# Kernel tuning notes

Measured on AMD Instinct MI355X. Metric: run time of the kernel, lower is better.

The kernel has to match this reference:

```python
import jax, jax.numpy as jnp
import numpy as np
from jax import lax

B, W, S, D, H, BH, C = 32, 128, 192, 768, 10, 30, 50
NEG = -1e30  # stand-in for -inf to keep grads NaN-free


def _lstm_dir(x, Wih, Whh, bih, bhh, reverse):
    # x: [B, T, D] -> [B, T, H]; torch gate order i, f, g, o
    xg = jnp.einsum('btd,gd->btg', x, Wih) + bih  # [B, T, 4H]
    if reverse:
        xg = xg[:, ::-1]

    def step(carry, g_t):
        h, c = carry
        g = g_t + h @ Whh.T + bhh
        i, f, gg, o = jnp.split(g, 4, axis=-1)
        c = jax.nn.sigmoid(f) * c + jax.nn.sigmoid(i) * jnp.tanh(gg)
        h = jax.nn.sigmoid(o) * jnp.tanh(c)
        return (h, c), h

    init = (jnp.zeros((x.shape[0], H), x.dtype), jnp.zeros((x.shape[0], H), x.dtype))
    _, hs = lax.scan(step, init, xg.transpose(1, 0, 2))
    hs = hs.transpose(1, 0, 2)
    if reverse:
        hs = hs[:, ::-1]
    return hs


def _biaffine(x, W1, b1, W2, b2, U, bias):
    # DeepBiaffineScorer: MLP+ReLU on each side, bilinear with bias-augmented inputs
    h1 = jax.nn.relu(x @ W1 + b1)
    h2 = jax.nn.relu(x @ W2 + b2)
    ones = jnp.ones(h1.shape[:-1] + (1,), h1.dtype)
    h1a = jnp.concatenate([h1, ones], -1)  # [B, W, BH+1]
    h2a = jnp.concatenate([h2, ones], -1)
    return jnp.einsum('bih,ohg,bjg->bijo', h1a, U, h2a) + bias  # [B, W, W, O]


def _ce_sum(logits, targets, ignore):
    # cross-entropy, reduction='sum', with ignore_index; classes on last axis
    logp = jax.nn.log_softmax(logits, -1)
    valid = targets != ignore
    t = jnp.where(valid, targets, 0)
    picked = jnp.take_along_axis(logp, t[..., None], -1).squeeze(-1)
    return -jnp.sum(jnp.where(valid, picked, 0.0))


def _forward(hiddens, bert2toks, heads, dep_rels, masks,
             Wih_f, Whh_f, bih_f, bhh_f, Wih_b, Whh_b, bih_b, bhh_b,
             un_W1, un_b1, un_W2, un_b2, un_U, un_bias,
             dr_W1, dr_b1, dr_W2, dr_b2, dr_U, dr_bias):
    # mean of the 3 selected BERT layers, then ragged subtoken -> word mean pooling
    means = jnp.mean(hiddens, axis=0)  # [B, S+1, D]
    sub = means[:, 1:]                 # skip [CLS]: [B, S, D]
    seg_sum = jax.vmap(lambda x, s: jax.ops.segment_sum(x, s, num_segments=W))(sub, bert2toks)
    cnt = jax.vmap(lambda s: jax.ops.segment_sum(jnp.ones((S,), sub.dtype), s, num_segments=W))(bert2toks)
    bert_out = seg_sum / jnp.maximum(cnt, 1.0)[..., None]  # [B, W, D]

    # BiLSTM (sent_lens are all full length W, so packing is the identity)
    fwd = _lstm_dir(bert_out, Wih_f, Whh_f, bih_f, bhh_f, False)
    bwd = _lstm_dir(bert_out, Wih_b, Whh_b, bih_b, bhh_b, True)
    unpacked = jnp.concatenate([fwd, bwd], -1)  # [B, W, 2H]

    unlabeled = _biaffine(unpacked, un_W1, un_b1, un_W2, un_b2, un_U, un_bias)[..., 0]  # [B, W, W]
    deprel = _biaffine(unpacked, dr_W1, dr_b1, dr_W2, dr_b2, dr_U, dr_bias)             # [B, W, W, C]

    eye = jnp.eye(W, dtype=bool)
    unlabeled = jnp.where(eye[None], NEG, unlabeled)

    # gather gold-head deprel scores: [B, W, C]
    head_scores = jnp.take_along_axis(deprel, heads[:, :, None, None], axis=2).squeeze(2)
    heads_ = jnp.where(masks, -1, heads)

    deprel_loss = _ce_sum(head_scores, dep_rels, 0)
    depind_loss = _ce_sum(unlabeled[:, 1:], heads_[:, 1:], -1)
    return deprel_loss + depind_loss


def setup_inputs() -> dict:
    key = jax.random.key(0)
    ks = jax.random.split(key, 26)
    hiddens = jax.random.normal(ks[0], (3, B, S + 1, D), jnp.float32)
    # non-decreasing subtoken->word map covering all W words
    bert2toks = jnp.broadcast_to((jnp.arange(S) * W) // S, (B, S)).astype(jnp.int32)
    heads = jax.random.randint(ks[1], (B, W), 0, W)
    heads = jnp.where(heads == jnp.arange(W)[None, :], 0, heads)  # no self-head (diag is -inf)
    dep_rels = jax.random.randint(ks[2], (B, W), 0, C)
    masks = jnp.zeros((B, W), bool)
    sent_lens = jnp.full((B,), W, jnp.int32)
    s = 0.1
    p = lambda k, shape: jax.random.normal(k, shape, jnp.float32) * s
    return dict(
        hiddens=hiddens, bert2toks=bert2toks, heads=heads, dep_rels=dep_rels,
        masks=masks, sent_lens=sent_lens,
        Wih_f=p(ks[3], (4 * H, D)), Whh_f=p(ks[4], (4 * H, H)), bih_f=p(ks[5], (4 * H,)), bhh_f=p(ks[6], (4 * H,)),
        Wih_b=p(ks[7], (4 * H, D)), Whh_b=p(ks[8], (4 * H, H)), bih_b=p(ks[9], (4 * H,)), bhh_b=p(ks[10], (4 * H,)),
        un_W1=p(ks[11], (2 * H, BH)), un_b1=p(ks[12], (BH,)), un_W2=p(ks[13], (2 * H, BH)), un_b2=p(ks[14], (BH,)),
        un_U=p(ks[15], (1, BH + 1, BH + 1)), un_bias=p(ks[16], (1,)),
        dr_W1=p(ks[17], (2 * H, BH)), dr_b1=p(ks[18], (BH,)), dr_W2=p(ks[19], (2 * H, BH)), dr_b2=p(ks[20], (BH,)),
        dr_U=p(ks[21], (C, BH + 1, BH + 1)), dr_bias=p(ks[22], (C,)),
    )


def reference(hiddens, bert2toks, heads, dep_rels, masks, sent_lens,
              Wih_f, Whh_f, bih_f, bhh_f, Wih_b, Whh_b, bih_b, bhh_b,
              un_W1, un_b1, un_W2, un_b2, un_U, un_bias,
              dr_W1, dr_b1, dr_W2, dr_b2, dr_U, dr_bias):
    # sent_lens unused: all sentences are full length, so pack/unpack is identity
    return _forward(hiddens, bert2toks, heads, dep_rels, masks,
                    Wih_f, Whh_f, bih_f, bhh_f, Wih_b, Whh_b, bih_b, bhh_b,
                    un_W1, un_b1, un_W2, un_b2, un_U, un_bias,
                    dr_W1, dr_b1, dr_W2, dr_b2, dr_U, dr_bias)
```

## Files before the change

kernel.cpp:

```cpp
#include <hip/hip_runtime.h>

#define Bn 32
#define Wn 128
#define Sn 192
#define Dn 768
#define Hn 10
#define BHn 30
#define Cn 50
#define CAP 8
#define NEGV -1e30f

__device__ __forceinline__ float fsig(float x) {
    return __builtin_amdgcn_rcpf(1.0f + __expf(-x));
}
__device__ __forceinline__ float ftanh(float x) {
    return 1.0f - 2.0f * __builtin_amdgcn_rcpf(1.0f + __expf(2.0f * x));
}
__device__ __forceinline__ float lane_bcast(float v, int srclane) {
    union { float f; int i; } u, w;
    u.f = v;
    w.i = __builtin_amdgcn_readlane(u.i, srclane);
    return w.f;
}
template <int Q>
__device__ __forceinline__ float quad_bcast(float v) {
    union { float f; int i; } u, w;
    u.f = v;
    w.i = __builtin_amdgcn_mov_dpp(u.i, (Q << 6) | (Q << 4) | (Q << 2) | Q, 0xf, 0xf, true);
    return w.f;
}

__global__ void k_zero(int* cnt, float* out) {
    int i = blockIdx.x * blockDim.x + threadIdx.x;
    if (i < Bn * Wn) cnt[i] = 0;
    if (i == 0) out[0] = 0.f;
}

__global__ void k_lists(const int* __restrict__ b2t, int* cnt, int* lists) {
    int idx = blockIdx.x * blockDim.x + threadIdx.x;
    if (idx >= Bn * Sn) return;
    int b = idx / Sn;
    int w = b2t[idx];
    if (w < 0 || w >= Wn) return;
    int s = idx % Sn;
    int pos = atomicAdd(&cnt[b * Wn + w], 1);
    if (pos < CAP) lists[(b * Wn + w) * CAP + pos] = s;
}

#define XSTR 100
#define WSTR 52
__global__ __launch_bounds__(256) void k_tokproj(const float* __restrict__ hid,
                                                 const float* __restrict__ Wf,
                                                 const float* __restrict__ Wb,
                                                 float* __restrict__ tokg4) {
    __shared__ float xl[64 * XSTR];
    __shared__ float wl[80 * WSTR];
    int tb = blockIdx.x >> 3;
    int kq = blockIdx.x & 7;
    int b = tb / 3;
    int s0 = (tb % 3) * 64;
    int k0 = kq * 96;
    int tid = threadIdx.x;

    for (int idx = tid; idx < 64 * 24; idx += 256) {
        int r = idx / 24, k4 = idx % 24;
        size_t rowbase = ((size_t)b * (Sn + 1) + (s0 + r + 1)) * Dn + k0 + 4 * k4;
        float4 v0 = *(const float4*)(hid + rowbase);
        float4 v1 = *(const float4*)(hid + (size_t)Bn * (Sn + 1) * Dn + rowbase);
        float4 v2 = *(const float4*)(hid + (size_t)2 * Bn * (Sn + 1) * Dn + rowbase);
        float4 v;
        v.x = v0.x + v1.x + v2.x; v.y = v0.y + v1.y + v2.y;
        v.z = v0.z + v1.z + v2.z; v.w = v0.w + v1.w + v2.w;
        *(float4*)(xl + r * XSTR + 4 * k4) = v;
    }

    int tg = tid >> 4;
    int rg = tid & 15;
    float acc[4][5];
#pragma unroll
    for (int tt = 0; tt < 4; ++tt)
#pragma unroll
        for (int rr = 0; rr < 5; ++rr) acc[tt][rr] = 0.f;

    for (int c = 0; c < 2; ++c) {
        __syncthreads();
        for (int idx = tid; idx < 80 * 12; idx += 256) {
            int co = idx / 12, k4c = idx % 12;
            int dir = co / 40, off = co % 40;
            int j = off >> 2, g = off & 3;
            const float* src = (dir ? Wb : Wf) + (g * 10 + j) * Dn + k0 + c * 48 + 4 * k4c;
            *(float4*)(wl + co * WSTR + 4 * k4c) = *(const float4*)src;
        }
        __syncthreads();
#pragma unroll 2
        for (int k4c = 0; k4c < 12; ++k4c) {
            float4 xv[4], wv[5];
#pragma unroll
            for (int tt = 0; tt < 4; ++tt)
                xv[tt] = *(const float4*)(xl + (tg * 4 + tt) * XSTR + c * 48 + 4 * k4c);
#pragma unroll
            for (int rr = 0; rr < 5; ++rr)
                wv[rr] = *(const float4*)(wl + (rg * 5 + rr) * WSTR + 4 * k4c);
#pragma unroll
            for (int tt = 0; tt < 4; ++tt)
#pragma unroll
                for (int rr = 0; rr < 5; ++rr) {
                    acc[tt][rr] += xv[tt].x * wv[rr].x + xv[tt].y * wv[rr].y
                                 + xv[tt].z * wv[rr].z + xv[tt].w * wv[rr].w;
                }
        }
    }
    size_t nbase = (size_t)kq * (Bn * Sn) + (size_t)b * Sn + s0;
#pragma unroll
    for (int tt = 0; tt < 4; ++tt) {
        size_t ob = (nbase + tg * 4 + tt) * 80 + rg * 5;
#pragma unroll
        for (int rr = 0; rr < 5; ++rr) tokg4[ob + rr] = acc[tt][rr];
    }
}

__global__ __launch_bounds__(128) void k_wordmean(const float* __restrict__ tokg4,
                                                  const int* __restrict__ cnt,
                                                  const int* __restrict__ lists,
                                                  const float* __restrict__ bih_f,
                                                  const float* __restrict__ bih_b,
                                                  float* __restrict__ xg) {
    const size_t NT80 = (size_t)Bn * Sn * 80;
    int bw = blockIdx.x;
    int b = bw / Wn, w = bw % Wn;
    int l = threadIdx.x;
    if (l >= 80) return;
    int dir = l / 40, off = l % 40;
    int c = cnt[bw];
    int cc = c < CAP ? c : CAP;
    float acc = 0.f;
    for (int tk = 0; tk < cc; ++tk) {
        int s = lists[bw * CAP + tk];
        size_t base = ((size_t)b * Sn + s) * 80 + l;
#pragma unroll
        for (int p = 0; p < 8; ++p) acc += tokg4[base + p * NT80];
    }
    float inv = 1.0f / (3.0f * (float)(c > 0 ? c : 1));
    int brow = (off & 3) * 10 + (off >> 2);
    float bias = (dir ? bih_b : bih_f)[brow];
    xg[((size_t)(dir * Bn + b) * Wn + w) * 40 + off] = acc * inv + bias;
}

__global__ __launch_bounds__(64) void k_lstm(const float* __restrict__ xg,
                                             const float* __restrict__ Whh_f, const float* __restrict__ bhh_f,
                                             const float* __restrict__ Whh_b, const float* __restrict__ bhh_b,
                                             float* __restrict__ hs) {
    int lane = threadIdx.x;
    int seq = blockIdx.x;
    int dir = seq >> 5;
    int l = lane < 40 ? lane : 39;
    int j = l >> 2, G = l & 3;

    const float* Whh = dir ? Whh_b : Whh_f;
    const float* bhh = dir ? bhh_b : bhh_f;
    float wk[Hn];
#pragma unroll
    for (int k = 0; k < Hn; ++k) wk[k] = Whh[(G * Hn + j) * Hn + k];
    float bias = bhh[G * Hn + j];

    const float* xbase = xg + (size_t)seq * Wn * 40;
    float* hbase = hs + (size_t)seq * Wn * Hn;
    bool st = (G == 0) && (lane < 40);

    float h = 0.f, c = 0.f;
    int dt = dir ? -1 : 1;
    int t = dir ? (Wn - 1) : 0;
    float xq[4];
    xq[0] = xbase[t * 40 + l];
    xq[1] = xbase[(t + dt) * 40 + l];
    xq[2] = xbase[(t + 2 * dt) * 40 + l];

#pragma unroll 4
    for (int step = 0; step < Wn; ++step) {
        float xv = xq[step & 3];
        xq[(step + 3) & 3] = xbase[(t + 3 * dt) * 40 + l];
        float hb[Hn];
#pragma unroll
        for (int k = 0; k < Hn; ++k) hb[k] = lane_bcast(h, 4 * k);
        float ga = xv, gb = bias;
#pragma unroll
        for (int k = 0; k < 5; ++k) ga += wk[k] * hb[k];
#pragma unroll
        for (int k = 5; k < Hn; ++k) gb += wk[k] * hb[k];
        float g = ga + gb;
        float gin = (G == 2) ? 2.f * g : g;
        float s = fsig(gin);
        float av = (G == 2) ? 2.f * s - 1.f : s;
        float ai = quad_bcast<0>(av);
        float af = quad_bcast<1>(av);
        float ag = quad_bcast<2>(av);
        float ao = quad_bcast<3>(av);
        c = af * c + ai * ag;
        h = ao * ftanh(c);
        if (st) hbase[t * Hn + j] = h;
        t += dt;
    }
}

__global__ __launch_bounds__(128) void k_mlp(const float* __restrict__ hs,
                                             const float* __restrict__ uW1, const float* __restrict__ ub1,
                                             const float* __restrict__ uW2, const float* __restrict__ ub2,
                                             const float* __restrict__ dW1, const float* __restrict__ db1,
                                             const float* __restrict__ dW2, const float* __restrict__ db2,
                                             float* __restrict__ hpad) {
    int bt = blockIdx.x;
    int b = bt / Wn, t = bt % Wn;
    __shared__ float x[20];
    int tid = threadIdx.x;
    if (tid < 20) {
        x[tid] = (tid < Hn) ? hs[((size_t)(0 * Bn + b) * Wn + t) * Hn + tid]
                            : hs[((size_t)(1 * Bn + b) * Wn + t) * Hn + (tid - Hn)];
    }
    __syncthreads();
    if (tid >= 124) {
        hpad[((size_t)(tid - 124) * Bn * Wn + bt) * 32 + 31] = 0.f;
        return;
    }
    int which = tid / 31, k = tid % 31;
    float v;
    if (k == 30) {
        v = 1.0f;
    } else {
        const float* Wm;
        const float* bv;
        if (which == 0) { Wm = uW1; bv = ub1; }
        else if (which == 1) { Wm = uW2; bv = ub2; }
        else if (which == 2) { Wm = dW1; bv = db1; }
        else { Wm = dW2; bv = db2; }
        float a = bv[k];
#pragma unroll
        for (int d = 0; d < 20; ++d) a += x[d] * Wm[d * BHn + k];
        v = a > 0.f ? a : 0.f;
    }
    hpad[((size_t)which * Bn * Wn + bt) * 32 + k] = v;
}

__global__ __launch_bounds__(256) void k_gather(const float* __restrict__ hpad,
                                                const int* __restrict__ heads,
                                                float* __restrict__ h2g) {
    int idx = blockIdx.x * 256 + threadIdx.x;
    int n = idx >> 3, q = idx & 7;
    int b = n >> 7;
    int jh = heads[n];
    if (jh < 0 || jh >= Wn) jh = 0;
    const float4* src = (const float4*)(hpad + ((size_t)3 * Bn * Wn + b * Wn + jh) * 32);
    ((float4*)(h2g + (size_t)n * 32))[q] = src[q];
}

__global__ __launch_bounds__(256) void k_drscore(const float* __restrict__ h1g,
                                                 const float* __restrict__ h2g,
                                                 const float* __restrict__ U, const float* __restrict__ dbias,
                                                 float* __restrict__ sc) {
    int nc = blockIdx.x & 63;
    int oq = blockIdx.x >> 6;
    __shared__ float Ul[4][992];
    int tid = threadIdx.x;
    for (int idx = tid; idx < 4 * 992; idx += 256) {
        int o = idx / 992, r = idx - o * 992;
        int h = r >> 5, g = r & 31;
        int oo = oq * 4 + o; if (oo >= Cn) oo = Cn - 1;
        Ul[o][r] = (g < 31) ? U[(size_t)oo * 961 + h * 31 + g] : 0.f;
    }
    int w = tid >> 6, lane = tid & 63;
    int o = oq * 4 + w;
    int n = nc * 64 + lane;
    float h2r[32];
    {
        const float4* p = (const float4*)(h2g + (size_t)n * 32);
#pragma unroll
        for (int q = 0; q < 8; ++q) {
            float4 v = p[q];
            h2r[4 * q + 0] = v.x; h2r[4 * q + 1] = v.y;
            h2r[4 * q + 2] = v.z; h2r[4 * q + 3] = v.w;
        }
    }
    float h1r[32];
    {
        const float4* p = (const float4*)(h1g + (size_t)n * 32);
#pragma unroll
        for (int q = 0; q < 8; ++q) {
            float4 v = p[q];
            h1r[4 * q + 0] = v.x; h1r[4 * q + 1] = v.y;
            h1r[4 * q + 2] = v.z; h1r[4 * q + 3] = v.w;
        }
    }
    __syncthreads();
    const float* up = Ul[w];
    float acc = 0.f;
    for (int h = 0; h < 31; ++h) {
        float t = 0.f;
#pragma unroll
        for (int g = 0; g < 32; ++g) t += up[h * 32 + g] * h2r[g];
        acc += h1r[h] * t;
    }
    if (o < Cn) sc[(size_t)n * Cn + o] = acc + dbias[o];
}

__global__ __launch_bounds__(256) void k_loss2(const float* __restrict__ hpad,
                                               const float* __restrict__ U0, const float* __restrict__ ubias,
                                               const float* __restrict__ sc,
                                               const int* __restrict__ heads,
                                               const unsigned char* __restrict__ masks,
                                               const int* __restrict__ dep_rels,
                                               float* __restrict__ out) {
    int b = blockIdx.x >> 2;
    int ic = blockIdx.x & 3;
    int tid = threadIdx.x;
    __shared__ float h2s[128 * 36];
    __shared__ float tg[32 * 36];
    __shared__ float U0l[992];
    __shared__ float red[256];
    const float* h1a = hpad + (size_t)b * Wn * 32;
    const float* h2a = hpad + ((size_t)Bn * Wn + b * Wn) * 32;
    for (int idx = tid; idx < 128 * 32; idx += 256)
        h2s[(idx >> 5) * 36 + (idx & 31)] = h2a[idx];
    for (int idx = tid; idx < 992; idx += 256) {
        int g = idx & 31;
        U0l[idx] = (g < 31) ? U0[(idx >> 5) * 31 + g] : 0.f;
    }
    __syncthreads();
    {
        int l = tid & 31, ig = tid >> 5;
        float ur[31];
#pragma unroll
        for (int h = 0; h < 31; ++h) ur[h] = U0l[h * 32 + l];
        for (int ii = 0; ii < 4; ++ii) {
            int il = ig * 4 + ii;
            int i = ic * 32 + il;
            const float4* hp = (const float4*)(h1a + (size_t)i * 32);
            float hr[32];
#pragma unroll
            for (int q = 0; q < 8; ++q) {
                float4 v = hp[q];
                hr[4 * q] = v.x; hr[4 * q + 1] = v.y; hr[4 * q + 2] = v.z; hr[4 * q + 3] = v.w;
            }
            float a = 0.f;
#pragma unroll
            for (int h = 0; h < 31; ++h) a += hr[h] * ur[h];
            tg[il * 36 + l] = a;
        }
    }
    __syncthreads();
    float acc = 0.f;
    {
        int jg = tid & 7, il = tid >> 3;
        int i = ic * 32 + il;
        float ub = ubias[0];
        float4 tq[8];
        const float4* tp = (const float4*)(tg + il * 36);
#pragma unroll
        for (int q = 0; q < 8; ++q) tq[q] = tp[q];
        float m = -3e38f, lsum = 0.f, sh = 0.f;
        int hd = heads[b * Wn + i];
        for (int jj = 0; jj < 16; ++jj) {
            int j = jg * 16 + ((jj + jg) & 15);
            const float4* h2p = (const float4*)(h2s + j * 36);
            float s = ub;
#pragma unroll
            for (int q = 0; q < 8; ++q) {
                float4 hq = h2p[q];
                s += tq[q].x * hq.x + tq[q].y * hq.y + tq[q].z * hq.z + tq[q].w * hq.w;
            }
            if (j == i) s = NEGV;
            float mn = fmaxf(m, s);
            lsum = lsum * __expf(m - mn) + __expf(s - mn);
            m = mn;
            if (j == hd) sh = s;
        }
        float shv = (jg == (hd >> 4)) ? sh : 0.f;
        float mm = m, ll = lsum;
#pragma unroll
        for (int off = 1; off < 8; off <<= 1) {
            float m2 = __shfl_xor(mm, off);
            float l2 = __shfl_xor(ll, off);
            float mn = fmaxf(mm, m2);
            ll = ll * __expf(mm - mn) + l2 * __expf(m2 - mn);
            mm = mn;
            shv += __shfl_xor(shv, off);
        }
        if (jg == 0 && i >= 1 && !masks[b * Wn + i])
            acc += -(shv - (mm + __logf(ll)));
    }
    if (tid < 32) {
        int n = b * Wn + ic * 32 + tid;
        int r = dep_rels[n];
        if (r != 0 && r < Cn) {
            const float* sp = sc + (size_t)n * Cn;
            float mm = sp[0];
            for (int o = 1; o < Cn; ++o) mm = fmaxf(mm, sp[o]);
            float e = 0.f;
            for (int o = 0; o < Cn; ++o) e += __expf(sp[o] - mm);
            acc += -(sp[r] - (mm + __logf(e)));
        }
    }
    red[tid] = acc;
    __syncthreads();
    for (int off = 128; off > 0; off >>= 1) {
        if (tid < off) red[tid] += red[tid + off];
        __syncthreads();
    }
    if (tid == 0) atomicAdd(out, red[0]);
}

extern "C" void kernel_launch(void* const* d_in, const int* in_sizes, int n_in,
                              void* d_out, int out_size, void* d_ws, size_t ws_size,
                              hipStream_t stream) {
    const float* hiddens = (const float*)d_in[0];
    const int* b2t = (const int*)d_in[1];
    const int* heads = (const int*)d_in[2];
    const int* dep_rels = (const int*)d_in[3];
    const unsigned char* masks = (const unsigned char*)d_in[4];
    const float* Wih_f = (const float*)d_in[6];
    const float* Whh_f = (const float*)d_in[7];
    const float* bih_f = (const float*)d_in[8];
    const float* bhh_f = (const float*)d_in[9];
    const float* Wih_b = (const float*)d_in[10];
    const float* Whh_b = (const float*)d_in[11];
    const float* bih_b = (const float*)d_in[12];
    const float* bhh_b = (const float*)d_in[13];
    const float* un_W1 = (const float*)d_in[14];
    const float* un_b1 = (const float*)d_in[15];
    const float* un_W2 = (const float*)d_in[16];
    const float* un_b2 = (const float*)d_in[17];
    const float* un_U  = (const float*)d_in[18];
    const float* un_bias = (const float*)d_in[19];
    const float* dr_W1 = (const float*)d_in[20];
    const float* dr_b1 = (const float*)d_in[21];
    const float* dr_W2 = (const float*)d_in[22];
    const float* dr_b2 = (const float*)d_in[23];
    const float* dr_U  = (const float*)d_in[24];
    const float* dr_bias = (const float*)d_in[25];

    char* p = (char*)d_ws;
    int* cnt = (int*)p;           p += (size_t)Bn * Wn * 4;
    int* lists = (int*)p;         p += (size_t)Bn * Wn * CAP * 4;
    float* tokg4 = (float*)p;     p += (size_t)8 * Bn * Sn * 80 * 4;
    float* xg = (float*)p;        p += (size_t)2 * Bn * Wn * 40 * 4;
    float* hs = (float*)p;        p += (size_t)2 * Bn * Wn * Hn * 4;
    float* hpad = (float*)p;      p += (size_t)4 * Bn * Wn * 32 * 4;
    float* h2g = (float*)p;       p += (size_t)Bn * Wn * 32 * 4;
    float* sc = (float*)p;        p += (size_t)Bn * Wn * Cn * 4;

    float* out = (float*)d_out;

    k_zero<<<(Bn * Wn + 255) / 256, 256, 0, stream>>>(cnt, out);
    k_lists<<<(Bn * Sn + 255) / 256, 256, 0, stream>>>(b2t, cnt, lists);
    k_tokproj<<<96 * 8, 256, 0, stream>>>(hiddens, Wih_f, Wih_b, tokg4);
    k_wordmean<<<Bn * Wn, 128, 0, stream>>>(tokg4, cnt, lists, bih_f, bih_b, xg);
    k_lstm<<<64, 64, 0, stream>>>(xg, Whh_f, bhh_f, Whh_b, bhh_b, hs);
    k_mlp<<<Bn * Wn, 128, 0, stream>>>(hs, un_W1, un_b1, un_W2, un_b2,
                                       dr_W1, dr_b1, dr_W2, dr_b2, hpad);
    k_gather<<<Bn * Wn * 8 / 256, 256, 0, stream>>>(hpad, heads, h2g);
    k_drscore<<<13 * 64, 256, 0, stream>>>(hpad + (size_t)2 * Bn * Wn * 32, h2g, dr_U, dr_bias, sc);
    k_loss2<<<Bn * 4, 256, 0, stream>>>(hpad, un_U, un_bias, sc, heads, masks, dep_rels, out);
}
```

Before: 100.9 us.

## Drop list-building and gather kernels, fuse into wordmean/drscore, retile tokproj

Removes the zero, list-building and gather kernels. Word mean pooling now scans the sentence's subtoken-to-word map from shared memory, and the dependency-relation scorer reads the head-gathered rows directly from hpad. Zeroing of the output moves into the projection kernel. The projection kernel is retiled to 128 threads with 8 token rows per thread and an XOR-swizzled shared layout to avoid bank conflicts. The goal is to cut launch count and intermediate traffic, at the cost of each wordmean block scanning all 192 subtokens.

```diff
diff --git a/kernel.cpp b/kernel.cpp
--- a/kernel.cpp
+++ b/kernel.cpp
@@ -7,7 +7,6 @@
 #define Hn 10
 #define BHn 30
 #define Cn 50
-#define CAP 8
 #define NEGV -1e30f
 
 __device__ __forceinline__ float fsig(float x) {
@@ -30,29 +29,13 @@
     return w.f;
 }
 
-__global__ void k_zero(int* cnt, float* out) {
-    int i = blockIdx.x * blockDim.x + threadIdx.x;
-    if (i < Bn * Wn) cnt[i] = 0;
-    if (i == 0) out[0] = 0.f;
-}
-
-__global__ void k_lists(const int* __restrict__ b2t, int* cnt, int* lists) {
-    int idx = blockIdx.x * blockDim.x + threadIdx.x;
-    if (idx >= Bn * Sn) return;
-    int b = idx / Sn;
-    int w = b2t[idx];
-    if (w < 0 || w >= Wn) return;
-    int s = idx % Sn;
-    int pos = atomicAdd(&cnt[b * Wn + w], 1);
-    if (pos < CAP) lists[(b * Wn + w) * CAP + pos] = s;
-}
-
-#define XSTR 100
+#define XSTR 96
 #define WSTR 52
-__global__ __launch_bounds__(256) void k_tokproj(const float* __restrict__ hid,
+__global__ __launch_bounds__(128) void k_tokproj(const float* __restrict__ hid,
                                                  const float* __restrict__ Wf,
                                                  const float* __restrict__ Wb,
-                                                 float* __restrict__ tokg4) {
+                                                 float* __restrict__ tokg4,
+                                                 float* __restrict__ out) {
     __shared__ float xl[64 * XSTR];
     __shared__ float wl[80 * WSTR];
     int tb = blockIdx.x >> 3;
@@ -61,8 +44,9 @@
     int s0 = (tb % 3) * 64;
     int k0 = kq * 96;
     int tid = threadIdx.x;
-
-    for (int idx = tid; idx < 64 * 24; idx += 256) {
+    if (blockIdx.x == 0 && tid == 0) out[0] = 0.f;
+
+    for (int idx = tid; idx < 64 * 24; idx += 128) {
         int r = idx / 24, k4 = idx % 24;
         size_t rowbase = ((size_t)b * (Sn + 1) + (s0 + r + 1)) * Dn + k0 + 4 * k4;
         float4 v0 = *(const float4*)(hid + rowbase);
@@ -71,20 +55,21 @@
         float4 v;
         v.x = v0.x + v1.x + v2.x; v.y = v0.y + v1.y + v2.y;
         v.z = v0.z + v1.z + v2.z; v.w = v0.w + v1.w + v2.w;
-        *(float4*)(xl + r * XSTR + 4 * k4) = v;
+        int slot = k4 ^ ((r >> 3) & 7);
+        *(float4*)(xl + r * XSTR + 4 * slot) = v;
     }
 
     int tg = tid >> 4;
     int rg = tid & 15;
-    float acc[4][5];
-#pragma unroll
-    for (int tt = 0; tt < 4; ++tt)
+    float acc[8][5];
+#pragma unroll
+    for (int tt = 0; tt < 8; ++tt)
 #pragma unroll
         for (int rr = 0; rr < 5; ++rr) acc[tt][rr] = 0.f;
 
     for (int c = 0; c < 2; ++c) {
         __syncthreads();
-        for (int idx = tid; idx < 80 * 12; idx += 256) {
+        for (int idx = tid; idx < 80 * 12; idx += 128) {
             int co = idx / 12, k4c = idx % 12;
             int dir = co / 40, off = co % 40;
             int j = off >> 2, g = off & 3;
@@ -94,15 +79,16 @@
         __syncthreads();
 #pragma unroll 2
         for (int k4c = 0; k4c < 12; ++k4c) {
-            float4 xv[4], wv[5];
-#pragma unroll
-            for (int tt = 0; tt < 4; ++tt)
-                xv[tt] = *(const float4*)(xl + (tg * 4 + tt) * XSTR + c * 48 + 4 * k4c);
+            int k4g = c * 12 + k4c;
+            float4 xv[8], wv[5];
+#pragma unroll
+            for (int tt = 0; tt < 8; ++tt)
+                xv[tt] = *(const float4*)(xl + (tg * 8 + tt) * XSTR + 4 * (k4g ^ tg));
 #pragma unroll
             for (int rr = 0; rr < 5; ++rr)
                 wv[rr] = *(const float4*)(wl + (rg * 5 + rr) * WSTR + 4 * k4c);
 #pragma unroll
-            for (int tt = 0; tt < 4; ++tt)
+            for (int tt = 0; tt < 8; ++tt)
 #pragma unroll
                 for (int rr = 0; rr < 5; ++rr) {
                     acc[tt][rr] += xv[tt].x * wv[rr].x + xv[tt].y * wv[rr].y
@@ -112,35 +98,39 @@
     }
     size_t nbase = (size_t)kq * (Bn * Sn) + (size_t)b * Sn + s0;
 #pragma unroll
-    for (int tt = 0; tt < 4; ++tt) {
-        size_t ob = (nbase + tg * 4 + tt) * 80 + rg * 5;
+    for (int tt = 0; tt < 8; ++tt) {
+        size_t ob = (nbase + tg * 8 + tt) * 80 + rg * 5;
 #pragma unroll
         for (int rr = 0; rr < 5; ++rr) tokg4[ob + rr] = acc[tt][rr];
     }
 }
 
-__global__ __launch_bounds__(128) void k_wordmean(const float* __restrict__ tokg4,
-                                                  const int* __restrict__ cnt,
-                                                  const int* __restrict__ lists,
-                                                  const float* __restrict__ bih_f,
-                                                  const float* __restrict__ bih_b,
-                                                  float* __restrict__ xg) {
+__global__ __launch_bounds__(96) void k_wordmean(const float* __restrict__ tokg4,
+                                                 const int* __restrict__ b2t,
+                                                 const float* __restrict__ bih_f,
+                                                 const float* __restrict__ bih_b,
+                                                 float* __restrict__ xg) {
     const size_t NT80 = (size_t)Bn * Sn * 80;
     int bw = blockIdx.x;
-    int b = bw / Wn, w = bw % Wn;
-    int l = threadIdx.x;
-    if (l >= 80) return;
-    int dir = l / 40, off = l % 40;
-    int c = cnt[bw];
-    int cc = c < CAP ? c : CAP;
+    int b = bw >> 7, w = bw & 127;
+    int tid = threadIdx.x;
+    __shared__ int ws[Sn];
+    ws[tid] = b2t[b * Sn + tid];
+    ws[96 + tid] = b2t[b * Sn + 96 + tid];
+    __syncthreads();
+    if (tid >= 80) return;
+    int dir = tid / 40, off = tid % 40;
     float acc = 0.f;
-    for (int tk = 0; tk < cc; ++tk) {
-        int s = lists[bw * CAP + tk];
-        size_t base = ((size_t)b * Sn + s) * 80 + l;
-#pragma unroll
-        for (int p = 0; p < 8; ++p) acc += tokg4[base + p * NT80];
-    }
-    float inv = 1.0f / (3.0f * (float)(c > 0 ? c : 1));
+    int cnt = 0;
+    for (int s = 0; s < Sn; ++s) {
+        if (ws[s] == w) {
+            ++cnt;
+            size_t base = ((size_t)b * Sn + s) * 80 + tid;
+#pragma unroll
+            for (int p = 0; p < 8; ++p) acc += tokg4[base + p * NT80];
+        }
+    }
+    float inv = 1.0f / (3.0f * (float)(cnt > 0 ? cnt : 1));
     int brow = (off & 3) * 10 + (off >> 2);
     float bias = (dir ? bih_b : bih_f)[brow];
     xg[((size_t)(dir * Bn + b) * Wn + w) * 40 + off] = acc * inv + bias;
@@ -240,20 +230,8 @@
     hpad[((size_t)which * Bn * Wn + bt) * 32 + k] = v;
 }
 
-__global__ __launch_bounds__(256) void k_gather(const float* __restrict__ hpad,
-                                                const int* __restrict__ heads,
-                                                float* __restrict__ h2g) {
-    int idx = blockIdx.x * 256 + threadIdx.x;
-    int n = idx >> 3, q = idx & 7;
-    int b = n >> 7;
-    int jh = heads[n];
-    if (jh < 0 || jh >= Wn) jh = 0;
-    const float4* src = (const float4*)(hpad + ((size_t)3 * Bn * Wn + b * Wn + jh) * 32);
-    ((float4*)(h2g + (size_t)n * 32))[q] = src[q];
-}
-
-__global__ __launch_bounds__(256) void k_drscore(const float* __restrict__ h1g,
-                                                 const float* __restrict__ h2g,
+__global__ __launch_bounds__(256) void k_drscore(const float* __restrict__ hpad,
+                                                 const int* __restrict__ heads,
                                                  const float* __restrict__ U, const float* __restrict__ dbias,
                                                  float* __restrict__ sc) {
     int nc = blockIdx.x & 63;
@@ -269,9 +247,14 @@
     int w = tid >> 6, lane = tid & 63;
     int o = oq * 4 + w;
     int n = nc * 64 + lane;
+    int b = n >> 7;
+    int jh = heads[n];
+    if (jh < 0 || jh >= Wn) jh = 0;
+    const float* h1a = hpad + ((size_t)2 * Bn * Wn + n) * 32;
+    const float* h2a = hpad + ((size_t)3 * Bn * Wn + b * Wn + jh) * 32;
     float h2r[32];
     {
-        const float4* p = (const float4*)(h2g + (size_t)n * 32);
+        const float4* p = (const float4*)h2a;
 #pragma unroll
         for (int q = 0; q < 8; ++q) {
             float4 v = p[q];
@@ -281,7 +264,7 @@
     }
     float h1r[32];
     {
-        const float4* p = (const float4*)(h1g + (size_t)n * 32);
+        const float4* p = (const float4*)h1a;
 #pragma unroll
         for (int q = 0; q < 8; ++q) {
             float4 v = p[q];
@@ -437,25 +420,19 @@
     const float* dr_bias = (const float*)d_in[25];
 
     char* p = (char*)d_ws;
-    int* cnt = (int*)p;           p += (size_t)Bn * Wn * 4;
-    int* lists = (int*)p;         p += (size_t)Bn * Wn * CAP * 4;
     float* tokg4 = (float*)p;     p += (size_t)8 * Bn * Sn * 80 * 4;
     float* xg = (float*)p;        p += (size_t)2 * Bn * Wn * 40 * 4;
     float* hs = (float*)p;        p += (size_t)2 * Bn * Wn * Hn * 4;
     float* hpad = (float*)p;      p += (size_t)4 * Bn * Wn * 32 * 4;
-    float* h2g = (float*)p;       p += (size_t)Bn * Wn * 32 * 4;
     float* sc = (float*)p;        p += (size_t)Bn * Wn * Cn * 4;
 
     float* out = (float*)d_out;
 
-    k_zero<<<(Bn * Wn + 255) / 256, 256, 0, stream>>>(cnt, out);
-    k_lists<<<(Bn * Sn + 255) / 256, 256, 0, stream>>>(b2t, cnt, lists);
-    k_tokproj<<<96 * 8, 256, 0, stream>>>(hiddens, Wih_f, Wih_b, tokg4);
-    k_wordmean<<<Bn * Wn, 128, 0, stream>>>(tokg4, cnt, lists, bih_f, bih_b, xg);
+    k_tokproj<<<96 * 8, 128, 0, stream>>>(hiddens, Wih_f, Wih_b, tokg4, out);
+    k_wordmean<<<Bn * Wn, 96, 0, stream>>>(tokg4, b2t, bih_f, bih_b, xg);
     k_lstm<<<64, 64, 0, stream>>>(xg, Whh_f, bhh_f, Whh_b, bhh_b, hs);
     k_mlp<<<Bn * Wn, 128, 0, stream>>>(hs, un_W1, un_b1, un_W2, un_b2,
                                        dr_W1, dr_b1, dr_W2, dr_b2, hpad);
-    k_gather<<<Bn * Wn * 8 / 256, 256, 0, stream>>>(hpad, heads, h2g);
-    k_drscore<<<13 * 64, 256, 0, stream>>>(hpad + (size_t)2 * Bn * Wn * 32, h2g, dr_U, dr_bias, sc);
+    k_drscore<<<13 * 64, 256, 0, stream>>>(hpad, heads, dr_U, dr_bias, sc);
     k_loss2<<<Bn * 4, 256, 0, stream>>>(hpad, un_U, un_bias, sc, heads, masks, dep_rels, out);
 }
```

New measurement: 104.9 us. 4.0% more time.
